# Kernel optimization log

Measured on AMD Instinct MI355X. Metric: run time of the kernel, lower is better.

## Reference

```python
import jax, jax.numpy as jnp
import numpy as np

N, P, T, K = 20000, 5, 16, 3
IN, H, O = 150, 64, 128


def setup_inputs() -> dict:
    key = jax.random.key(0)
    k1, k2, k3, k4, k5 = jax.random.split(key, 5)
    x = jax.random.normal(k1, (N, IN), dtype=jnp.float32)
    conn_idx = jax.random.randint(k2, (N, P, T, K), 0, N, dtype=jnp.int32)
    conn_w = jax.random.uniform(k3, (N, P, T, K), dtype=jnp.float32)
    # learned params
    W1 = jax.random.normal(k4, (H, IN), dtype=jnp.float32) * 0.05   # linear_1 (no bias)
    Wg = jax.random.normal(k5, (O, H, P, T), dtype=jnp.float32) * 0.05  # geodesic conv weight
    bg = jnp.zeros((O,), dtype=jnp.float32)                          # geodesic conv bias
    return {"x": x, "conn_idx": conn_idx, "conn_w": conn_w, "W1": W1, "Wg": Wg, "bg": bg}


def reference(x, conn_idx, conn_w, W1, Wg, bg):
    # Linear + ReLU: [N, H]
    h = jax.nn.relu(x @ W1.T)
    # Geodesic patch gather: interpolate vertex features into P x T bins
    g = jnp.take(h, conn_idx, axis=0)                 # [N, P, T, K, H]
    patches = jnp.einsum('nptk,nptkh->npth', conn_w, g)  # [N, P, T, H]
    # Geodesic convolution: contract patch bins and channels
    out = jnp.einsum('npth,ohpt->no', patches, Wg) + bg  # [N, O]
    # L2 normalize per vertex
    norm = jnp.linalg.norm(out, axis=-1, keepdims=True)
    return out / norm
```

## Files before the change

kernel.cpp:

```cpp
#include <hip/hip_runtime.h>
#include <hip/hip_fp16.h>

#define NV   20000
#define KK   3
#define INF  150
#define HH   64
#define OO   128
#define PT   80
#define KTOT 5120
#define NB   160
#define RS   72
#define CB   (NB * RS)
#define XS   168
#define NBIN 20
#define NCH  10

typedef _Float16 fh8 __attribute__((ext_vector_type(8)));
typedef __attribute__((ext_vector_type(4))) float f32x4;
typedef __attribute__((ext_vector_type(8))) unsigned short u16x8;

__device__ __forceinline__ unsigned short f2h(float f) {
    return __half_as_ushort(__float2half(f));
}
__device__ __forceinline__ float h2f(unsigned short u) {
    return __half2float(__ushort_as_half(u));
}
__device__ __forceinline__ _Float16 u2h(unsigned short u) {
    union { unsigned short s; _Float16 h; } c; c.s = u; return c.h;
}

__global__ __launch_bounds__(256) void prep_kernel(
    const float* __restrict__ Wg, const float* __restrict__ x,
    const float* __restrict__ W1, unsigned short* __restrict__ W2,
    unsigned short* __restrict__ hb) {
    __shared__ __align__(16) unsigned char smem[32256];
    const int tid = threadIdx.x;

    if (blockIdx.x < 128) {
        float* lds = (float*)smem;
        const int o = blockIdx.x;
        const float* src = Wg + o * KTOT;
        for (int e = tid; e < KTOT / 4; e += 256) {
            const float4 v4 = ((const float4*)src)[e];
            const int t = e * 4;
            const int h = t / 80, bin = t - h * 80;
            lds[h * 81 + bin]     = v4.x;
            lds[h * 81 + bin + 1] = v4.y;
            lds[h * 81 + bin + 2] = v4.z;
            lds[h * 81 + bin + 3] = v4.w;
        }
        __syncthreads();
        for (int e = tid; e < KTOT / 2; e += 256) {
            const int t = e * 2;
            const unsigned int h0 = f2h(lds[(t & 63) * 81 + (t >> 6)]);
            const unsigned int h1 = f2h(lds[((t + 1) & 63) * 81 + ((t + 1) >> 6)]);
            *(unsigned int*)(W2 + (t >> 5) * 4096 + o * 32 + (t & 31)) =
                h0 | (h1 << 16);
        }
        return;
    }

    unsigned short* xs = (unsigned short*)smem;
    unsigned short* ws = xs + 32 * XS;
    const int n0 = (blockIdx.x - 128) * 32;

    {
        const float2* x2 = (const float2*)(x + (size_t)n0 * INF);
        for (int e = tid; e < 32 * (INF / 2); e += 256) {
            const int f = e * 2;
            const int r = f / INF, c = f - r * INF;
            const float2 v = x2[e];
            const unsigned int p =
                (unsigned int)f2h(v.x) | ((unsigned int)f2h(v.y) << 16);
            *(unsigned int*)(xs + r * XS + c) = p;
        }
    }
    for (int e = tid; e < 32 * 9; e += 256) {
        const int r = e / 9, c2 = e - r * 9;
        *(unsigned int*)(xs + r * XS + 150 + c2 * 2) = 0;
    }
    {
        const float2* w2p = (const float2*)W1;
        for (int e = tid; e < 64 * (INF / 2); e += 256) {
            const int f = e * 2;
            const int r = f / INF, c = f - r * INF;
            const float2 v = w2p[e];
            const unsigned int p =
                (unsigned int)f2h(v.x) | ((unsigned int)f2h(v.y) << 16);
            *(unsigned int*)(ws + r * XS + c) = p;
        }
    }
    for (int e = tid; e < 64 * 9; e += 256) {
        const int r = e / 9, c2 = e - r * 9;
        *(unsigned int*)(ws + r * XS + 150 + c2 * 2) = 0;
    }
    __syncthreads();

    const int wv   = tid >> 6;
    const int lane = tid & 63;
    const int q    = lane >> 4;
    const int r16  = lane & 15;
    const int o0   = wv * 16;

    f32x4 acc0 = {0.f, 0.f, 0.f, 0.f};
    f32x4 acc1 = acc0;
    #pragma unroll
    for (int s = 0; s < 5; s++) {
        const int kb = s * 32 + q * 8;
        fh8 a0 = *(const fh8*)(xs + r16 * XS + kb);
        fh8 a1 = *(const fh8*)(xs + (16 + r16) * XS + kb);
        fh8 b  = *(const fh8*)(ws + (o0 + r16) * XS + kb);
        acc0 = __builtin_amdgcn_mfma_f32_16x16x32_f16(a0, b, acc0, 0, 0, 0);
        acc1 = __builtin_amdgcn_mfma_f32_16x16x32_f16(a1, b, acc1, 0, 0, 0);
    }
    #pragma unroll
    for (int r = 0; r < 4; r++) {
        float v0 = acc0[r] > 0.f ? acc0[r] : 0.f;
        float v1 = acc1[r] > 0.f ? acc1[r] : 0.f;
        hb[(n0 + q * 4 + r) * HH + o0 + r16]      = f2h(v0);
        hb[(n0 + 16 + q * 4 + r) * HH + o0 + r16] = f2h(v1);
    }
}

__global__ __launch_bounds__(512, 4) void geo_kernel(
    const int*   __restrict__ conn_idx, const float* __restrict__ conn_w,
    const unsigned short* __restrict__ W2, const unsigned short* __restrict__ hb,
    float* __restrict__ out, unsigned short* __restrict__ parts) {
    __shared__ __align__(16) unsigned short pch[2 * CB];
    __shared__ __align__(16) unsigned short cp[NB * NCH * 8];

    const int tid  = threadIdx.x;
    const int ks   = blockIdx.x & 3;
    const int n0   = (blockIdx.x >> 2) * NB;
    const int wv   = tid >> 6;
    const int lane = tid & 63;
    const int q    = lane >> 4;
    const int r16  = lane & 15;
    const int j8   = tid & 7;
    const int v0   = tid >> 3;
    const bool lo  = (tid < 256);
    const int bbase = ks * NBIN;
    const int Sbase = ks * 40;

    for (int e = tid; e < NB * NCH; e += 512) {
        const int v = e / NCH, cc = e - v * NCH;
        const int g = (n0 + v) * (PT * KK) + (bbase + cc) * KK;
        u16x8 pk;
        pk[0] = (unsigned short)conn_idx[g];
        pk[1] = (unsigned short)conn_idx[g + 1];
        pk[2] = (unsigned short)conn_idx[g + 2];
        pk[3] = f2h(conn_w[g]);
        pk[4] = f2h(conn_w[g + 1]);
        pk[5] = f2h(conn_w[g + 2]);
        pk[6] = 0; pk[7] = 0;
        *(u16x8*)(cp + e * 8) = pk;
    }

    u16x8 cpre0, cpre1, cpre2, cpre3 = {0, 0, 0, 0, 0, 0, 0, 0};
    {
        auto packc = [&](int e) {
            const int v = e / NCH, cc = e - v * NCH;
            const int g = (n0 + v) * (PT * KK) + (bbase + NCH + cc) * KK;
            u16x8 pk;
            pk[0] = (unsigned short)conn_idx[g];
            pk[1] = (unsigned short)conn_idx[g + 1];
            pk[2] = (unsigned short)conn_idx[g + 2];
            pk[3] = f2h(conn_w[g]);
            pk[4] = f2h(conn_w[g + 1]);
            pk[5] = f2h(conn_w[g + 2]);
            pk[6] = 0; pk[7] = 0;
            return pk;
        };
        cpre0 = packc(tid);
        cpre1 = packc(tid + 512);
        cpre2 = packc(tid + 1024);
        if (tid < NB * NCH - 1536) cpre3 = packc(tid + 1536);
    }

    f32x4 acc[10];
    #pragma unroll
    for (int m = 0; m < 10; m++) acc[m] = (f32x4){0.f, 0.f, 0.f, 0.f};

    u16x8 pa, pb, pc;
    fh8   hva0, hva1, hva2, hvb0, hvb1, hvb2, hvc0, hvc1, hvc2;

    auto loadg = [&](int cc) {
        const int bb = (cc >= NCH) ? cc - NCH : cc;
        pa = *(const u16x8*)(cp + (v0 * NCH + bb) * 8);
        pb = *(const u16x8*)(cp + ((v0 + 64) * NCH + bb) * 8);
        hva0 = *(const fh8*)(hb + (int)pa[0] * HH + j8 * 8);
        hva1 = *(const fh8*)(hb + (int)pa[1] * HH + j8 * 8);
        hva2 = *(const fh8*)(hb + (int)pa[2] * HH + j8 * 8);
        hvb0 = *(const fh8*)(hb + (int)pb[0] * HH + j8 * 8);
        hvb1 = *(const fh8*)(hb + (int)pb[1] * HH + j8 * 8);
        hvb2 = *(const fh8*)(hb + (int)pb[2] * HH + j8 * 8);
        if (lo) {
            pc = *(const u16x8*)(cp + ((v0 + 128) * NCH + bb) * 8);
            hvc0 = *(const fh8*)(hb + (int)pc[0] * HH + j8 * 8);
            hvc1 = *(const fh8*)(hb + (int)pc[1] * HH + j8 * 8);
            hvc2 = *(const fh8*)(hb + (int)pc[2] * HH + j8 * 8);
        }
    };
    auto cwr = [&](unsigned short* buf) {
        const _Float16 a0 = u2h(pa[3]), a1 = u2h(pa[4]), a2 = u2h(pa[5]);
        const _Float16 b0 = u2h(pb[3]), b1 = u2h(pb[4]), b2 = u2h(pb[5]);
        const fh8 A0 = {a0, a0, a0, a0, a0, a0, a0, a0};
        const fh8 A1 = {a1, a1, a1, a1, a1, a1, a1, a1};
        const fh8 A2 = {a2, a2, a2, a2, a2, a2, a2, a2};
        const fh8 B0 = {b0, b0, b0, b0, b0, b0, b0, b0};
        const fh8 B1 = {b1, b1, b1, b1, b1, b1, b1, b1};
        const fh8 B2 = {b2, b2, b2, b2, b2, b2, b2, b2};
        fh8 ra = hva0 * A0 + hva1 * A1 + hva2 * A2;
        fh8 rb = hvb0 * B0 + hvb1 * B1 + hvb2 * B2;
        *(fh8*)(buf + v0 * RS + j8 * 8)        = ra;
        *(fh8*)(buf + (v0 + 64) * RS + j8 * 8) = rb;
        if (lo) {
            const _Float16 c0 = u2h(pc[3]), c1 = u2h(pc[4]), c2 = u2h(pc[5]);
            const fh8 C0 = {c0, c0, c0, c0, c0, c0, c0, c0};
            const fh8 C1 = {c1, c1, c1, c1, c1, c1, c1, c1};
            const fh8 C2 = {c2, c2, c2, c2, c2, c2, c2, c2};
            fh8 rc = hvc0 * C0 + hvc1 * C1 + hvc2 * C2;
            *(fh8*)(buf + (v0 + 128) * RS + j8 * 8) = rc;
        }
    };
    auto mfmaph = [&](const unsigned short* buf, int cc) {
        const unsigned short* wp =
            W2 + (Sbase + cc * 2) * 4096 + (wv * 16 + r16) * 32 + q * 8;
        const fh8 bf0 = *(const fh8*)(wp);
        const fh8 bf1 = *(const fh8*)(wp + 4096);
        #pragma unroll
        for (int s = 0; s < 2; s++) {
            const int ao = s * 32 + q * 8;
            const fh8 bf = s ? bf1 : bf0;
            #pragma unroll
            for (int m = 0; m < 10; m++) {
                fh8 af = *(const fh8*)(buf + (m * 16 + r16) * RS + ao);
                acc[m] = __builtin_amdgcn_mfma_f32_16x16x32_f16(af, bf, acc[m], 0, 0, 0);
            }
        }
    };

    __syncthreads();

    loadg(0);
    cwr(pch);
    __syncthreads();

    #pragma unroll 1
    for (int cc = 0; cc < NBIN; cc++) {
        if (cc == NCH - 1) {
            *(u16x8*)(cp + tid * 8)          = cpre0;
            *(u16x8*)(cp + (tid + 512) * 8)  = cpre1;
            *(u16x8*)(cp + (tid + 1024) * 8) = cpre2;
            if (tid < NB * NCH - 1536)
                *(u16x8*)(cp + (tid + 1536) * 8) = cpre3;
            __syncthreads();
        }
        if (cc + 1 < NBIN) loadg(cc + 1);
        mfmaph(&pch[(cc & 1) * CB], cc);
        if (cc + 1 < NBIN) cwr(&pch[((cc + 1) & 1) * CB]);
        __syncthreads();
    }

    if (ks == 0) {
        #pragma unroll
        for (int m = 0; m < 10; m++) {
            const int rb = n0 + m * 16 + q * 4;
            #pragma unroll
            for (int r = 0; r < 4; r++)
                out[(rb + r) * OO + wv * 16 + r16] = acc[m][r];
        }
    } else {
        unsigned short* pp = parts + (ks - 1) * (NV * OO);
        #pragma unroll
        for (int m = 0; m < 10; m++) {
            const int rb = n0 + m * 16 + q * 4;
            #pragma unroll
            for (int r = 0; r < 4; r++)
                pp[(rb + r) * OO + wv * 16 + r16] = f2h(acc[m][r]);
        }
    }
}

__global__ __launch_bounds__(256) void norm_kernel(
    float* __restrict__ out, const unsigned short* __restrict__ parts,
    const float* __restrict__ bg) {
    const int tid  = threadIdx.x;
    const int n    = blockIdx.x * 32 + (tid >> 3);
    const int l    = tid & 7;
    const int base = n * OO + l * 16;

    float4 o4[4];
    #pragma unroll
    for (int i = 0; i < 4; i++)
        o4[i] = *(const float4*)(out + base + i * 4);

    u16x8 p[3][2];
    #pragma unroll
    for (int s = 0; s < 3; s++) {
        p[s][0] = *(const u16x8*)(parts + s * (NV * OO) + base);
        p[s][1] = *(const u16x8*)(parts + s * (NV * OO) + base + 8);
    }

    float4 b4[4];
    #pragma unroll
    for (int i = 0; i < 4; i++)
        b4[i] = *(const float4*)(bg + l * 16 + i * 4);

    float v[16];
    float s = 0.f;
    #pragma unroll
    for (int i = 0; i < 16; i++) {
        const float ov = (i & 3) == 0 ? o4[i >> 2].x :
                         (i & 3) == 1 ? o4[i >> 2].y :
                         (i & 3) == 2 ? o4[i >> 2].z : o4[i >> 2].w;
        const float bv = (i & 3) == 0 ? b4[i >> 2].x :
                         (i & 3) == 1 ? b4[i >> 2].y :
                         (i & 3) == 2 ? b4[i >> 2].z : b4[i >> 2].w;
        v[i] = ov + h2f(p[0][i >> 3][i & 7]) + h2f(p[1][i >> 3][i & 7]) +
               h2f(p[2][i >> 3][i & 7]) + bv;
        s += v[i] * v[i];
    }
    for (int off = 4; off; off >>= 1) s += __shfl_down(s, off, 8);
    const float r = rsqrtf(__shfl(s, 0, 8));
    #pragma unroll
    for (int i = 0; i < 4; i++) {
        float4 w = {v[i * 4] * r, v[i * 4 + 1] * r,
                    v[i * 4 + 2] * r, v[i * 4 + 3] * r};
        *(float4*)(out + base + i * 4) = w;
    }
}

extern "C" void kernel_launch(void* const* d_in, const int* in_sizes, int n_in,
                              void* d_out, int out_size, void* d_ws, size_t ws_size,
                              hipStream_t stream) {
    const float* x        = (const float*)d_in[0];
    const int*   conn_idx = (const int*)  d_in[1];
    const float* conn_w   = (const float*)d_in[2];
    const float* W1       = (const float*)d_in[3];
    const float* Wg       = (const float*)d_in[4];
    const float* bg       = (const float*)d_in[5];
    float*       out      = (float*)d_out;

    unsigned short* W2    = (unsigned short*)d_ws;
    unsigned short* hb    = W2 + OO * KTOT;
    unsigned short* parts = hb + NV * HH;

    hipLaunchKernelGGL(prep_kernel, dim3(128 + NV / 32), dim3(256), 0, stream,
                       Wg, x, W1, W2, hb);
    hipLaunchKernelGGL(geo_kernel, dim3(4 * (NV / NB)), dim3(512), 0, stream,
                       conn_idx, conn_w, W2, hb, out, parts);
    hipLaunchKernelGGL(norm_kernel, dim3(NV / 32), dim3(256), 0, stream,
                       out, parts, bg);
}
```

Before: 162.1 us.

## Drop split-K partials and fuse bias plus L2 normalization into geo kernel

Stops splitting the 80-bin reduction across four blocks. Each block now processes 80 vertices over all bins and computes bias, row norms and the normalized output in an LDS reduction epilogue, so the fp16 partial buffers and the separate norm kernel are removed. This saves one launch, the partial-buffer writes and reads, and the fp16 rounding of partials. In exchange the grid shrinks to 250 blocks with a longer serial loop of 80 steps, occupancy bounds drop to 2, and each block stages all 80 bins of connectivity in LDS.

Result: slower. 185.7 us (+14.5%).

```diff
diff --git a/kernel.cpp b/kernel.cpp
--- a/kernel.cpp
+++ b/kernel.cpp
@@ -8,12 +8,11 @@
 #define OO   128
 #define PT   80
 #define KTOT 5120
-#define NB   160
+#define NB   80
 #define RS   72
 #define CB   (NB * RS)
 #define XS   168
-#define NBIN 20
-#define NCH  10
+#define CPS  81
 
 typedef _Float16 fh8 __attribute__((ext_vector_type(8)));
 typedef __attribute__((ext_vector_type(4))) float f32x4;
@@ -21,9 +20,6 @@
 
 __device__ __forceinline__ unsigned short f2h(float f) {
     return __half_as_ushort(__float2half(f));
-}
-__device__ __forceinline__ float h2f(unsigned short u) {
-    return __half2float(__ushort_as_half(u));
 }
 __device__ __forceinline__ _Float16 u2h(unsigned short u) {
     union { unsigned short s; _Float16 h; } c; c.s = u; return c.h;
@@ -122,29 +118,26 @@
     }
 }
 
-__global__ __launch_bounds__(512, 4) void geo_kernel(
+__global__ __launch_bounds__(512, 2) void geo_kernel(
     const int*   __restrict__ conn_idx, const float* __restrict__ conn_w,
     const unsigned short* __restrict__ W2, const unsigned short* __restrict__ hb,
-    float* __restrict__ out, unsigned short* __restrict__ parts) {
+    const float* __restrict__ bg, float* __restrict__ out) {
     __shared__ __align__(16) unsigned short pch[2 * CB];
-    __shared__ __align__(16) unsigned short cp[NB * NCH * 8];
+    __shared__ __align__(16) unsigned short cp[NB * CPS * 8];
 
     const int tid  = threadIdx.x;
-    const int ks   = blockIdx.x & 3;
-    const int n0   = (blockIdx.x >> 2) * NB;
+    const int n0   = blockIdx.x * NB;
     const int wv   = tid >> 6;
     const int lane = tid & 63;
     const int q    = lane >> 4;
     const int r16  = lane & 15;
     const int j8   = tid & 7;
     const int v0   = tid >> 3;
-    const bool lo  = (tid < 256);
-    const int bbase = ks * NBIN;
-    const int Sbase = ks * 40;
-
-    for (int e = tid; e < NB * NCH; e += 512) {
-        const int v = e / NCH, cc = e - v * NCH;
-        const int g = (n0 + v) * (PT * KK) + (bbase + cc) * KK;
+    const bool lo  = (v0 < 16);
+
+    for (int e = tid; e < NB * 80; e += 512) {
+        const int v = e / 80, cc = e - v * 80;
+        const int g = (n0 + v) * (PT * KK) + cc * KK;
         u16x8 pk;
         pk[0] = (unsigned short)conn_idx[g];
         pk[1] = (unsigned short)conn_idx[g + 1];
@@ -153,49 +146,23 @@
         pk[4] = f2h(conn_w[g + 1]);
         pk[5] = f2h(conn_w[g + 2]);
         pk[6] = 0; pk[7] = 0;
-        *(u16x8*)(cp + e * 8) = pk;
-    }
-
-    u16x8 cpre0, cpre1, cpre2, cpre3 = {0, 0, 0, 0, 0, 0, 0, 0};
-    {
-        auto packc = [&](int e) {
-            const int v = e / NCH, cc = e - v * NCH;
-            const int g = (n0 + v) * (PT * KK) + (bbase + NCH + cc) * KK;
-            u16x8 pk;
-            pk[0] = (unsigned short)conn_idx[g];
-            pk[1] = (unsigned short)conn_idx[g + 1];
-            pk[2] = (unsigned short)conn_idx[g + 2];
-            pk[3] = f2h(conn_w[g]);
-            pk[4] = f2h(conn_w[g + 1]);
-            pk[5] = f2h(conn_w[g + 2]);
-            pk[6] = 0; pk[7] = 0;
-            return pk;
-        };
-        cpre0 = packc(tid);
-        cpre1 = packc(tid + 512);
-        cpre2 = packc(tid + 1024);
-        if (tid < NB * NCH - 1536) cpre3 = packc(tid + 1536);
-    }
-
-    f32x4 acc[10];
-    #pragma unroll
-    for (int m = 0; m < 10; m++) acc[m] = (f32x4){0.f, 0.f, 0.f, 0.f};
-
-    u16x8 pa, pb, pc;
-    fh8   hva0, hva1, hva2, hvb0, hvb1, hvb2, hvc0, hvc1, hvc2;
+        *(u16x8*)(cp + (v * CPS + cc) * 8) = pk;
+    }
+
+    f32x4 acc[5];
+    #pragma unroll
+    for (int m = 0; m < 5; m++) acc[m] = (f32x4){0.f, 0.f, 0.f, 0.f};
+
+    u16x8 pa, pc;
+    fh8   hva0, hva1, hva2, hvc0, hvc1, hvc2;
 
     auto loadg = [&](int cc) {
-        const int bb = (cc >= NCH) ? cc - NCH : cc;
-        pa = *(const u16x8*)(cp + (v0 * NCH + bb) * 8);
-        pb = *(const u16x8*)(cp + ((v0 + 64) * NCH + bb) * 8);
+        pa = *(const u16x8*)(cp + (v0 * CPS + cc) * 8);
         hva0 = *(const fh8*)(hb + (int)pa[0] * HH + j8 * 8);
         hva1 = *(const fh8*)(hb + (int)pa[1] * HH + j8 * 8);
         hva2 = *(const fh8*)(hb + (int)pa[2] * HH + j8 * 8);
-        hvb0 = *(const fh8*)(hb + (int)pb[0] * HH + j8 * 8);
-        hvb1 = *(const fh8*)(hb + (int)pb[1] * HH + j8 * 8);
-        hvb2 = *(const fh8*)(hb + (int)pb[2] * HH + j8 * 8);
         if (lo) {
-            pc = *(const u16x8*)(cp + ((v0 + 128) * NCH + bb) * 8);
+            pc = *(const u16x8*)(cp + ((v0 + 64) * CPS + cc) * 8);
             hvc0 = *(const fh8*)(hb + (int)pc[0] * HH + j8 * 8);
             hvc1 = *(const fh8*)(hb + (int)pc[1] * HH + j8 * 8);
             hvc2 = *(const fh8*)(hb + (int)pc[2] * HH + j8 * 8);
@@ -203,29 +170,23 @@
     };
     auto cwr = [&](unsigned short* buf) {
         const _Float16 a0 = u2h(pa[3]), a1 = u2h(pa[4]), a2 = u2h(pa[5]);
-        const _Float16 b0 = u2h(pb[3]), b1 = u2h(pb[4]), b2 = u2h(pb[5]);
         const fh8 A0 = {a0, a0, a0, a0, a0, a0, a0, a0};
         const fh8 A1 = {a1, a1, a1, a1, a1, a1, a1, a1};
         const fh8 A2 = {a2, a2, a2, a2, a2, a2, a2, a2};
-        const fh8 B0 = {b0, b0, b0, b0, b0, b0, b0, b0};
-        const fh8 B1 = {b1, b1, b1, b1, b1, b1, b1, b1};
-        const fh8 B2 = {b2, b2, b2, b2, b2, b2, b2, b2};
         fh8 ra = hva0 * A0 + hva1 * A1 + hva2 * A2;
-        fh8 rb = hvb0 * B0 + hvb1 * B1 + hvb2 * B2;
-        *(fh8*)(buf + v0 * RS + j8 * 8)        = ra;
-        *(fh8*)(buf + (v0 + 64) * RS + j8 * 8) = rb;
+        *(fh8*)(buf + v0 * RS + j8 * 8) = ra;
         if (lo) {
             const _Float16 c0 = u2h(pc[3]), c1 = u2h(pc[4]), c2 = u2h(pc[5]);
             const fh8 C0 = {c0, c0, c0, c0, c0, c0, c0, c0};
             const fh8 C1 = {c1, c1, c1, c1, c1, c1, c1, c1};
             const fh8 C2 = {c2, c2, c2, c2, c2, c2, c2, c2};
             fh8 rc = hvc0 * C0 + hvc1 * C1 + hvc2 * C2;
-            *(fh8*)(buf + (v0 + 128) * RS + j8 * 8) = rc;
+            *(fh8*)(buf + (v0 + 64) * RS + j8 * 8) = rc;
         }
     };
     auto mfmaph = [&](const unsigned short* buf, int cc) {
         const unsigned short* wp =
-            W2 + (Sbase + cc * 2) * 4096 + (wv * 16 + r16) * 32 + q * 8;
+            W2 + (cc * 2) * 4096 + (wv * 16 + r16) * 32 + q * 8;
         const fh8 bf0 = *(const fh8*)(wp);
         const fh8 bf1 = *(const fh8*)(wp + 4096);
         #pragma unroll
@@ -233,7 +194,7 @@
             const int ao = s * 32 + q * 8;
             const fh8 bf = s ? bf1 : bf0;
             #pragma unroll
-            for (int m = 0; m < 10; m++) {
+            for (int m = 0; m < 5; m++) {
                 fh8 af = *(const fh8*)(buf + (m * 16 + r16) * RS + ao);
                 acc[m] = __builtin_amdgcn_mfma_f32_16x16x32_f16(af, bf, acc[m], 0, 0, 0);
             }
@@ -247,87 +208,54 @@
     __syncthreads();
 
     #pragma unroll 1
-    for (int cc = 0; cc < NBIN; cc++) {
-        if (cc == NCH - 1) {
-            *(u16x8*)(cp + tid * 8)          = cpre0;
-            *(u16x8*)(cp + (tid + 512) * 8)  = cpre1;
-            *(u16x8*)(cp + (tid + 1024) * 8) = cpre2;
-            if (tid < NB * NCH - 1536)
-                *(u16x8*)(cp + (tid + 1536) * 8) = cpre3;
-            __syncthreads();
-        }
-        if (cc + 1 < NBIN) loadg(cc + 1);
+    for (int cc = 0; cc < 80; cc++) {
+        if (cc + 1 < 80) loadg(cc + 1);
         mfmaph(&pch[(cc & 1) * CB], cc);
-        if (cc + 1 < NBIN) cwr(&pch[((cc + 1) & 1) * CB]);
+        if (cc + 1 < 80) cwr(&pch[((cc + 1) & 1) * CB]);
         __syncthreads();
     }
 
-    if (ks == 0) {
-        #pragma unroll
-        for (int m = 0; m < 10; m++) {
-            const int rb = n0 + m * 16 + q * 4;
+    float* sums = (float*)pch;
+    float* rsy  = sums + NB * 33;
+
+    const float bias = bg[wv * 16 + r16];
+    float ps[5][4];
+    #pragma unroll
+    for (int m = 0; m < 5; m++) {
+        f32x4 v = acc[m];
+        v[0] += bias; v[1] += bias; v[2] += bias; v[3] += bias;
+        acc[m] = v;
+        #pragma unroll
+        for (int r = 0; r < 4; r++) {
+            float s2 = v[r] * v[r];
+            s2 += __shfl_xor(s2, 1, 16);
+            s2 += __shfl_xor(s2, 2, 16);
+            ps[m][r] = s2;
+        }
+    }
+    if ((r16 & 3) == 0) {
+        #pragma unroll
+        for (int m = 0; m < 5; m++)
             #pragma unroll
             for (int r = 0; r < 4; r++)
-                out[(rb + r) * OO + wv * 16 + r16] = acc[m][r];
-        }
-    } else {
-        unsigned short* pp = parts + (ks - 1) * (NV * OO);
-        #pragma unroll
-        for (int m = 0; m < 10; m++) {
-            const int rb = n0 + m * 16 + q * 4;
-            #pragma unroll
-            for (int r = 0; r < 4; r++)
-                pp[(rb + r) * OO + wv * 16 + r16] = f2h(acc[m][r]);
-        }
-    }
-}
-
-__global__ __launch_bounds__(256) void norm_kernel(
-    float* __restrict__ out, const unsigned short* __restrict__ parts,
-    const float* __restrict__ bg) {
-    const int tid  = threadIdx.x;
-    const int n    = blockIdx.x * 32 + (tid >> 3);
-    const int l    = tid & 7;
-    const int base = n * OO + l * 16;
-
-    float4 o4[4];
-    #pragma unroll
-    for (int i = 0; i < 4; i++)
-        o4[i] = *(const float4*)(out + base + i * 4);
-
-    u16x8 p[3][2];
-    #pragma unroll
-    for (int s = 0; s < 3; s++) {
-        p[s][0] = *(const u16x8*)(parts + s * (NV * OO) + base);
-        p[s][1] = *(const u16x8*)(parts + s * (NV * OO) + base + 8);
-    }
-
-    float4 b4[4];
-    #pragma unroll
-    for (int i = 0; i < 4; i++)
-        b4[i] = *(const float4*)(bg + l * 16 + i * 4);
-
-    float v[16];
-    float s = 0.f;
-    #pragma unroll
-    for (int i = 0; i < 16; i++) {
-        const float ov = (i & 3) == 0 ? o4[i >> 2].x :
-                         (i & 3) == 1 ? o4[i >> 2].y :
-                         (i & 3) == 2 ? o4[i >> 2].z : o4[i >> 2].w;
-        const float bv = (i & 3) == 0 ? b4[i >> 2].x :
-                         (i & 3) == 1 ? b4[i >> 2].y :
-                         (i & 3) == 2 ? b4[i >> 2].z : b4[i >> 2].w;
-        v[i] = ov + h2f(p[0][i >> 3][i & 7]) + h2f(p[1][i >> 3][i & 7]) +
-               h2f(p[2][i >> 3][i & 7]) + bv;
-        s += v[i] * v[i];
-    }
-    for (int off = 4; off; off >>= 1) s += __shfl_down(s, off, 8);
-    const float r = rsqrtf(__shfl(s, 0, 8));
-    #pragma unroll
-    for (int i = 0; i < 4; i++) {
-        float4 w = {v[i * 4] * r, v[i * 4 + 1] * r,
-                    v[i * 4 + 2] * r, v[i * 4 + 3] * r};
-        *(float4*)(out + base + i * 4) = w;
+                sums[(m * 16 + q * 4 + r) * 33 + wv * 4 + (r16 >> 2)] = ps[m][r];
+    }
+    __syncthreads();
+    if (tid < NB) {
+        float tot = 0.f;
+        #pragma unroll
+        for (int c = 0; c < 32; c++) tot += sums[tid * 33 + c];
+        rsy[tid] = rsqrtf(tot);
+    }
+    __syncthreads();
+    #pragma unroll
+    for (int m = 0; m < 5; m++) {
+        const int rb = n0 + m * 16 + q * 4;
+        #pragma unroll
+        for (int r = 0; r < 4; r++) {
+            const float rs = rsy[m * 16 + q * 4 + r];
+            out[(rb + r) * OO + wv * 16 + r16] = acc[m][r] * rs;
+        }
     }
 }
 
@@ -344,12 +272,9 @@
 
     unsigned short* W2    = (unsigned short*)d_ws;
     unsigned short* hb    = W2 + OO * KTOT;
-    unsigned short* parts = hb + NV * HH;
 
     hipLaunchKernelGGL(prep_kernel, dim3(128 + NV / 32), dim3(256), 0, stream,
                        Wg, x, W1, W2, hb);
-    hipLaunchKernelGGL(geo_kernel, dim3(4 * (NV / NB)), dim3(512), 0, stream,
-                       conn_idx, conn_w, W2, hb, out, parts);
-    hipLaunchKernelGGL(norm_kernel, dim3(NV / 32), dim3(256), 0, stream,
-                       out, parts, bg);
-}
+    hipLaunchKernelGGL(geo_kernel, dim3(NV / NB), dim3(512), 0, stream,
+                       conn_idx, conn_w, W2, hb, bg, out);
+}
```
